# Kernel optimization log

Hardware: AMD Instinct MI355X
Metric: run time of the kernel (lower is better)

## Reference

```python
import jax, jax.numpy as jnp
from jax import lax
import numpy as np

KSIZE = 5  # kernel_size from init
CHANNEL = 256

def _gaussian_kernel2d(sigma, ksize):
    # matches torch: exp(-i^2/(2*sigma^2)) outer product, normalized to sum 1
    n = ksize // 2
    r = jnp.arange(-n, n + 1, dtype=jnp.float32)
    g = jnp.exp(-(r ** 2) / (2.0 * sigma ** 2))
    k2d = g[:, None] * g[None, :]
    return k2d / k2d.sum()

def setup_inputs() -> dict:
    key = jax.random.key(0)
    k1, k2 = jax.random.split(key)
    x = jax.random.normal(k1, (16, CHANNEL, 64, 64), dtype=jnp.float32)
    # sigma is the module's learned scalar; keep away from 0 for a well-defined kernel
    sigma = jax.random.uniform(k2, (1,), dtype=jnp.float32, minval=0.5, maxval=1.5)
    return {"x": x, "sigma": sigma}

def reference(x, sigma):
    # The torch module writes a channel-diagonal weight into a dense Conv2d;
    # mathematically this is a depthwise conv with the same 2D Gaussian per channel.
    C = x.shape[1]
    k2d = _gaussian_kernel2d(sigma[0], KSIZE)
    w = jnp.broadcast_to(k2d[None, None, :, :], (C, 1, KSIZE, KSIZE))  # OIHW, groups=C
    pad = KSIZE // 2
    return lax.conv_general_dilated(
        x, w,
        window_strides=(1, 1),
        padding=[(pad, pad), (pad, pad)],
        dimension_numbers=("NCHW", "OIHW", "NCHW"),
        feature_group_count=C,
    )
```

## Files before the change

kernel.cpp:

```cpp
#include <hip/hip_runtime.h>
#include <math.h>


constexpr int Hh = 64;
constexpr int Ww = 64;
constexpr int KS = 5;
constexpr int PADc = 2;

__global__ __launch_bounds__(256, 2) void gauss5(const float* __restrict__ x,
                                                 const float* __restrict__ sigma,
                                                 float* __restrict__ out) {
    const int t    = threadIdx.x;
    const int lane = t & 63;
    const int wid  = t >> 6;
    const size_t plane = (size_t)blockIdx.x * 4 + wid;

    const int c4  = lane & 15;
    const int g16 = (lane >> 4) << 4;

    const float sg = sigma[0];
    const float c2 = -1.0f / (2.0f * sg * sg);
    float w[KS];
    float wsum = 0.0f;
#pragma unroll
    for (int i = 0; i < KS; ++i) {
        float d = (float)(i - PADc);
        w[i] = expf(d * d * c2);
        wsum += w[i];
    }
    const float winv = 1.0f / wsum;
#pragma unroll
    for (int i = 0; i < KS; ++i) w[i] *= winv;

    const float4* __restrict__ x4 = (const float4*)(x + plane * (Hh * Ww));
    float4* __restrict__ o4       = (float4*)(out + plane * (Hh * Ww));

    const int lm1 = lane - 1;
    const int lp1 = lane + 1;
    const bool leftEdge  = (c4 == 0);
    const bool rightEdge = (c4 == 15);

    float4 h[20];
#pragma unroll
    for (int i = 0; i < 20; ++i) {
        int ri = g16 - PADc + i;
        int rc = ri < 0 ? 0 : (ri > 63 ? 63 : ri);
        float4 v = x4[rc * 16 + c4];
        if (ri != rc) { v.x = 0.f; v.y = 0.f; v.z = 0.f; v.w = 0.f; }

        float lz = __shfl(v.z, lm1, 64);
        float lw = __shfl(v.w, lm1, 64);
        float rx = __shfl(v.x, lp1, 64);
        float ry = __shfl(v.y, lp1, 64);
        lz = leftEdge  ? 0.f : lz;
        lw = leftEdge  ? 0.f : lw;
        rx = rightEdge ? 0.f : rx;
        ry = rightEdge ? 0.f : ry;

        h[i].x = w[0]*lz  + w[1]*lw  + w[2]*v.x + w[3]*v.y + w[4]*v.z;
        h[i].y = w[0]*lw  + w[1]*v.x + w[2]*v.y + w[3]*v.z + w[4]*v.w;
        h[i].z = w[0]*v.x + w[1]*v.y + w[2]*v.z + w[3]*v.w + w[4]*rx;
        h[i].w = w[0]*v.y + w[1]*v.z + w[2]*v.w + w[3]*rx  + w[4]*ry;
    }

#pragma unroll
    for (int r = 0; r < 16; ++r) {
        float4 a;
        a.x = w[0]*h[r].x; a.y = w[0]*h[r].y; a.z = w[0]*h[r].z; a.w = w[0]*h[r].w;
#pragma unroll
        for (int j = 1; j < KS; ++j) {
            a.x += w[j] * h[r + j].x;
            a.y += w[j] * h[r + j].y;
            a.z += w[j] * h[r + j].z;
            a.w += w[j] * h[r + j].w;
        }
        o4[(g16 + r) * 16 + c4] = a;
    }
}

extern "C" void kernel_launch(void* const* d_in, const int* in_sizes, int n_in,
                              void* d_out, int out_size, void* d_ws, size_t ws_size,
                              hipStream_t stream) {
    const float* x     = (const float*)d_in[0];
    const float* sigma = (const float*)d_in[1];
    float* out         = (float*)d_out;
    const int planes = in_sizes[0] / (Hh * Ww);
    gauss5<<<planes / 4, 256, 0, stream>>>(x, sigma, out);
}
```

Baseline: 117.6 us.

## Exchange vertical halo rows via cross-group shuffles and use nontemporal loads/stores

Each 16-row group now loads only its own 16 rows instead of 20. The two halo rows above and below come from the horizontally filtered results of neighbouring lane groups through wave shuffles, and zeros are used at the plane edges. This removes the redundant halo reloads. Loads and stores become nontemporal, and all 16 loads are issued up front to increase memory-level parallelism. The cost is 16 extra shuffles per lane and more registers held live.

Result: slower. 125.1 us (+6.4%).

```diff
diff --git a/kernel.cpp b/kernel.cpp
--- a/kernel.cpp
+++ b/kernel.cpp
@@ -6,6 +6,8 @@
 constexpr int Ww = 64;
 constexpr int KS = 5;
 constexpr int PADc = 2;
+
+typedef float vf4 __attribute__((ext_vector_type(4)));
 
 __global__ __launch_bounds__(256, 2) void gauss5(const float* __restrict__ x,
                                                  const float* __restrict__ sigma,
@@ -16,7 +18,8 @@
     const size_t plane = (size_t)blockIdx.x * 4 + wid;
 
     const int c4  = lane & 15;
-    const int g16 = (lane >> 4) << 4;
+    const int grp = lane >> 4;
+    const int g16 = grp << 4;
 
     const float sg = sigma[0];
     const float c2 = -1.0f / (2.0f * sg * sg);
@@ -32,49 +35,71 @@
 #pragma unroll
     for (int i = 0; i < KS; ++i) w[i] *= winv;
 
-    const float4* __restrict__ x4 = (const float4*)(x + plane * (Hh * Ww));
-    float4* __restrict__ o4       = (float4*)(out + plane * (Hh * Ww));
+    const vf4* __restrict__ x4 = (const vf4*)(x + plane * (Hh * Ww));
+    vf4* __restrict__ o4       = (vf4*)(out + plane * (Hh * Ww));
 
     const int lm1 = lane - 1;
     const int lp1 = lane + 1;
     const bool leftEdge  = (c4 == 0);
     const bool rightEdge = (c4 == 15);
 
-    float4 h[20];
+    vf4 v[16];
 #pragma unroll
-    for (int i = 0; i < 20; ++i) {
-        int ri = g16 - PADc + i;
-        int rc = ri < 0 ? 0 : (ri > 63 ? 63 : ri);
-        float4 v = x4[rc * 16 + c4];
-        if (ri != rc) { v.x = 0.f; v.y = 0.f; v.z = 0.f; v.w = 0.f; }
+    for (int i = 0; i < 16; ++i)
+        v[i] = __builtin_nontemporal_load(&x4[(g16 + i) * 16 + c4]);
 
-        float lz = __shfl(v.z, lm1, 64);
-        float lw = __shfl(v.w, lm1, 64);
-        float rx = __shfl(v.x, lp1, 64);
-        float ry = __shfl(v.y, lp1, 64);
+    vf4 h[16];
+#pragma unroll
+    for (int i = 0; i < 16; ++i) {
+        vf4 a = v[i];
+        float lz = __shfl(a.z, lm1, 64);
+        float lw = __shfl(a.w, lm1, 64);
+        float rx = __shfl(a.x, lp1, 64);
+        float ry = __shfl(a.y, lp1, 64);
         lz = leftEdge  ? 0.f : lz;
         lw = leftEdge  ? 0.f : lw;
         rx = rightEdge ? 0.f : rx;
         ry = rightEdge ? 0.f : ry;
-
-        h[i].x = w[0]*lz  + w[1]*lw  + w[2]*v.x + w[3]*v.y + w[4]*v.z;
-        h[i].y = w[0]*lw  + w[1]*v.x + w[2]*v.y + w[3]*v.z + w[4]*v.w;
-        h[i].z = w[0]*v.x + w[1]*v.y + w[2]*v.z + w[3]*v.w + w[4]*rx;
-        h[i].w = w[0]*v.y + w[1]*v.z + w[2]*v.w + w[3]*rx  + w[4]*ry;
+        h[i].x = w[0]*lz  + w[1]*lw  + w[2]*a.x + w[3]*a.y + w[4]*a.z;
+        h[i].y = w[0]*lw  + w[1]*a.x + w[2]*a.y + w[3]*a.z + w[4]*a.w;
+        h[i].z = w[0]*a.x + w[1]*a.y + w[2]*a.z + w[3]*a.w + w[4]*rx;
+        h[i].w = w[0]*a.y + w[1]*a.z + w[2]*a.w + w[3]*rx  + w[4]*ry;
     }
 
+    const int lup = (lane + 48) & 63;
+    const int ldn = (lane + 16) & 63;
+    vf4 ha, hb, hc, hd;
+    ha.x = __shfl(h[14].x, lup, 64); ha.y = __shfl(h[14].y, lup, 64);
+    ha.z = __shfl(h[14].z, lup, 64); ha.w = __shfl(h[14].w, lup, 64);
+    hb.x = __shfl(h[15].x, lup, 64); hb.y = __shfl(h[15].y, lup, 64);
+    hb.z = __shfl(h[15].z, lup, 64); hb.w = __shfl(h[15].w, lup, 64);
+    hc.x = __shfl(h[0].x,  ldn, 64); hc.y = __shfl(h[0].y,  ldn, 64);
+    hc.z = __shfl(h[0].z,  ldn, 64); hc.w = __shfl(h[0].w,  ldn, 64);
+    hd.x = __shfl(h[1].x,  ldn, 64); hd.y = __shfl(h[1].y,  ldn, 64);
+    hd.z = __shfl(h[1].z,  ldn, 64); hd.w = __shfl(h[1].w,  ldn, 64);
+    if (grp == 0) { ha = 0.f; hb = 0.f; }
+    if (grp == 3) { hc = 0.f; hd = 0.f; }
+
+    {
+        vf4 a = w[0]*ha + w[1]*hb + w[2]*h[0] + w[3]*h[1] + w[4]*h[2];
+        __builtin_nontemporal_store(a, &o4[(g16 + 0) * 16 + c4]);
+    }
+    {
+        vf4 a = w[0]*hb + w[1]*h[0] + w[2]*h[1] + w[3]*h[2] + w[4]*h[3];
+        __builtin_nontemporal_store(a, &o4[(g16 + 1) * 16 + c4]);
+    }
 #pragma unroll
-    for (int r = 0; r < 16; ++r) {
-        float4 a;
-        a.x = w[0]*h[r].x; a.y = w[0]*h[r].y; a.z = w[0]*h[r].z; a.w = w[0]*h[r].w;
-#pragma unroll
-        for (int j = 1; j < KS; ++j) {
-            a.x += w[j] * h[r + j].x;
-            a.y += w[j] * h[r + j].y;
-            a.z += w[j] * h[r + j].z;
-            a.w += w[j] * h[r + j].w;
-        }
-        o4[(g16 + r) * 16 + c4] = a;
+    for (int r = 2; r <= 13; ++r) {
+        vf4 a = w[0]*h[r-2] + w[1]*h[r-1] + w[2]*h[r] + w[3]*h[r+1] + w[4]*h[r+2];
+        __builtin_nontemporal_store(a, &o4[(g16 + r) * 16 + c4]);
+    }
+    {
+        vf4 a = w[0]*h[12] + w[1]*h[13] + w[2]*h[14] + w[3]*h[15] + w[4]*hc;
+        __builtin_nontemporal_store(a, &o4[(g16 + 14) * 16 + c4]);
+    }
+    {
+        vf4 a = w[0]*h[13] + w[1]*h[14] + w[2]*h[15] + w[3]*hc + w[4]*hd;
+        __builtin_nontemporal_store(a, &o4[(g16 + 15) * 16 + c4]);
     }
 }
 
```
